# Kernel optimization log

Measured on AMD Instinct MI355X. Metric: run time of the kernel, lower is better.

## Reference

```python
import jax, jax.numpy as jnp
import numpy as np

B, D, H, F, L, M, MEM, ACT, STO, HID = 2048, 1024, 8, 4096, 2, 256, 16, 32, 1024, 1024
HD = D // H
SCALE = HD ** -0.5
EPS = 1e-4


def rmsnorm(x, w):
    return x * jax.lax.rsqrt(jnp.mean(x * x, axis=-1, keepdims=True) + EPS) * w


def setup_inputs() -> dict:
    key = jax.random.key(0)
    ks = iter(jax.random.split(key, 32))

    def nrm(shape, scale=0.02):
        return jax.random.normal(next(ks), shape, dtype=jnp.float32) * scale

    return {
        'stoch': jax.random.normal(next(ks), (B, STO), dtype=jnp.float32),
        'deter': jax.random.normal(next(ks), (B, D), dtype=jnp.float32),
        'action': jax.random.normal(next(ks), (B, ACT), dtype=jnp.float32),
        'memory': jax.random.normal(next(ks), (B, MEM, D), dtype=jnp.float32),
        'inp_w1': nrm((STO + ACT, HID)), 'inp_b1': jnp.zeros((HID,), jnp.float32),
        'inp_nw': jnp.ones((HID,), jnp.float32),
        'inp_w2': nrm((HID, D)), 'inp_b2': jnp.zeros((D,), jnp.float32),
        'Wq': nrm((L, D, D)), 'bq': jnp.zeros((L, D), jnp.float32),
        'Wk': nrm((L, D, D)), 'bk': jnp.zeros((L, D), jnp.float32),
        'Wv': nrm((L, D, D)), 'bv': jnp.zeros((L, D), jnp.float32),
        'Wo': nrm((L, D, D)), 'bo': jnp.zeros((L, D), jnp.float32),
        'rel_emb': nrm((L, 2 * M + 1, H)),
        'n1w': jnp.ones((L, D), jnp.float32), 'n2w': jnp.ones((L, D), jnp.float32),
        'ffw1': nrm((L, D, F)), 'ffb1': jnp.zeros((L, F), jnp.float32),
        'ffw2': nrm((L, F, D)), 'ffb2': jnp.zeros((L, D), jnp.float32),
        'fnw': jnp.ones((D,), jnp.float32),
    }


def reference(stoch, deter, action, memory, inp_w1, inp_b1, inp_nw, inp_w2, inp_b2,
              Wq, bq, Wk, bk, Wv, bv, Wo, bo, rel_emb, n1w, n2w,
              ffw1, ffb1, ffw2, ffb2, fnw):
    # action normalization: denominator is detached in torch
    a = action / jax.lax.stop_gradient(jnp.maximum(jnp.abs(action), 1.0))
    tok = jnp.concatenate([stoch.reshape(stoch.shape[0], -1), a], axis=-1)
    tok = jax.nn.silu(rmsnorm(tok @ inp_w1 + inp_b1, inp_nw)) @ inp_w2 + inp_b2  # [B,D]
    seq = jnp.concatenate([memory, tok[:, None, :]], axis=1)  # [B,S,D], S = MEM+1
    S = seq.shape[1]
    rel = jnp.clip(jnp.arange(S)[:, None] - jnp.arange(S)[None, :], -M, M) + M  # [S,S]
    for l in range(L):
        xn = rmsnorm(seq, n1w[l])
        q = (xn @ Wq[l] + bq[l]).reshape(-1, S, H, HD)
        k = (xn @ Wk[l] + bk[l]).reshape(-1, S, H, HD)
        v = (xn @ Wv[l] + bv[l]).reshape(-1, S, H, HD)
        bias = rel_emb[l][rel].transpose(2, 0, 1)  # [H,S,S]
        scores = jnp.einsum('bqhd,bkhd->bhqk', q, k) * SCALE + bias[None]
        probs = jax.nn.softmax(scores, axis=-1)
        att = jnp.einsum('bhqk,bkhd->bqhd', probs, v).reshape(-1, S, D)
        seq = seq + (att @ Wo[l] + bo[l])
        xn2 = rmsnorm(seq, n2w[l])
        seq = seq + (jax.nn.gelu(xn2 @ ffw1[l] + ffb1[l], approximate=False) @ ffw2[l] + ffb2[l])
    new_deter = rmsnorm(seq[:, -1] + deter, fnw)
    new_mem = jax.lax.stop_gradient(seq[:, -MEM:])
    return (new_deter, new_mem)
```

## Files before the change

kernel.cpp:

```cpp
#include <hip/hip_runtime.h>
#include <hip/hip_bf16.h>
#include <math.h>

#define NB 2048
#define ND 1024
#define NH 8
#define NHD 128
#define NF 4096
#define NL 2
#define NMEM 16
#define NS 17
#define NROWS (NB*NS)
#define NTOK 1056
#define SCALE_ATT 0.08838834764831845f

typedef unsigned short u16;
typedef unsigned int u32;

typedef __bf16 bf16x8 __attribute__((ext_vector_type(8)));
typedef float f32x4 __attribute__((ext_vector_type(4)));

__device__ __forceinline__ float bf2f(u16 h) {
  union { u32 u; float f; } c; c.u = ((u32)h) << 16; return c.f;
}
__device__ __forceinline__ u16 f2bf(float f) {
  union { float ff; u32 u; } c; c.ff = f;
  return (u16)((c.u + 0x7FFFu + ((c.u >> 16) & 1u)) >> 16);
}
__device__ __forceinline__ bf16x8 as_b8(uint4 u) {
  union { uint4 u; bf16x8 b; } c; c.u = u; return c.b;
}

__device__ __forceinline__ void gload16(const void* g, void* l) {
  __builtin_amdgcn_global_load_lds(
      (const __attribute__((address_space(1))) void*)(uintptr_t)g,
      (__attribute__((address_space(3))) void*)(u32)(uintptr_t)l,
      16, 0, 0);
}

__global__ __launch_bounds__(256)
void pack_wT_k(const float* __restrict__ src, u16* __restrict__ dst, int K, int N)
{
  __shared__ float tile[32][33];
  int tx = threadIdx.x & 31, ty = threadIdx.x >> 5;
  int n0 = blockIdx.x * 32, k0 = blockIdx.y * 32;
#pragma unroll
  for (int r = ty; r < 32; r += 8)
    tile[r][tx] = src[(size_t)(k0 + r) * N + n0 + tx];
  __syncthreads();
#pragma unroll
  for (int r = ty; r < 32; r += 8)
    dst[(size_t)(n0 + r) * K + k0 + tx] = f2bf(tile[tx][r]);
}

__global__ __launch_bounds__(256)
void pack_bqkv_k(const float* __restrict__ bq, const float* __restrict__ bk,
                 const float* __restrict__ bv, float* __restrict__ dst)
{
  int j = blockIdx.x * 256 + threadIdx.x;
  if (j >= 3072) return;
  float v = (j < 1024) ? bq[j] : (j < 2048 ? bk[j - 1024] : bv[j - 2048]);
  dst[j] = v;
}

template<int EPI>
__global__ __launch_bounds__(256)
void gemm2_k(const u16* __restrict__ A, int lda,
             const u16* __restrict__ BT, int ldb,
             const float* __restrict__ bias,
             u16* __restrict__ Cb, float* __restrict__ Cf, int ldc,
             int K)
{
  __shared__ __align__(16) u16 Asm[2][128 * 32];
  __shared__ __align__(16) u16 Bsm[2][128 * 32];
  const int tid  = threadIdx.x;
  const int lane = tid & 63;
  const int wv   = tid >> 6;
  const int wm   = wv >> 1, wn = wv & 1;
  const int lr   = lane & 15;
  const int kb   = lane >> 4;

  const int gx = gridDim.x;
  const int nwg = gx * gridDim.y;
  int bid = blockIdx.y * gx + blockIdx.x;
  if ((nwg & 7) == 0) bid = (bid & 7) * (nwg >> 3) + (bid >> 3);
  const int bx = bid % gx, by = bid / gx;
  const long bmBase = (long)by * 128;
  const int  bnBase = bx * 128;

  const int srow = tid >> 2;
  const int skc  = (tid & 3) * 8;
  const u16* aG0 = A  + (size_t)(bmBase + srow) * lda + skc;
  const u16* aG1 = aG0 + (size_t)64 * lda;
  const u16* bG0 = BT + (size_t)(bnBase + srow) * ldb + skc;
  const u16* bG1 = bG0 + (size_t)64 * ldb;
  const int wbase = (tid & ~63) * 8;

  f32x4 acc[4][4];
#pragma unroll
  for (int m = 0; m < 4; ++m)
#pragma unroll
    for (int n = 0; n < 4; ++n)
      acc[m][n] = (f32x4){0.0f, 0.0f, 0.0f, 0.0f};

  const int nk = K >> 5;

  {
    u16* aL = &Asm[0][wbase];
    u16* bL = &Bsm[0][wbase];
    gload16(aG0, aL);
    gload16(aG1, aL + 2048);
    gload16(bG0, bL);
    gload16(bG1, bL + 2048);
  }
  asm volatile("s_waitcnt vmcnt(0)" ::: "memory");
  __builtin_amdgcn_s_barrier();

  for (int i = 0; i < nk; ++i) {
    const int cur = i & 1;
    if (i + 1 < nk) {
      const int kt = (i + 1) << 5;
      u16* aL = &Asm[cur ^ 1][wbase];
      u16* bL = &Bsm[cur ^ 1][wbase];
      gload16(aG0 + kt, aL);
      gload16(aG1 + kt, aL + 2048);
      gload16(bG0 + kt, bL);
      gload16(bG1 + kt, bL + 2048);
    }

    bf16x8 af[4], bfv[4];
#pragma unroll
    for (int m = 0; m < 4; ++m)
      af[m] = as_b8(*(const uint4*)&Asm[cur][(wm * 64 + m * 16 + lr) * 32 + kb * 8]);
#pragma unroll
    for (int n = 0; n < 4; ++n)
      bfv[n] = as_b8(*(const uint4*)&Bsm[cur][(wn * 64 + n * 16 + lr) * 32 + kb * 8]);
#pragma unroll
    for (int m = 0; m < 4; ++m)
#pragma unroll
      for (int n = 0; n < 4; ++n)
        acc[m][n] = __builtin_amdgcn_mfma_f32_16x16x32_bf16(af[m], bfv[n], acc[m][n], 0, 0, 0);

    asm volatile("s_waitcnt vmcnt(0)" ::: "memory");
    __builtin_amdgcn_s_barrier();
  }

#pragma unroll
  for (int m = 0; m < 4; ++m) {
#pragma unroll
    for (int n = 0; n < 4; ++n) {
      int gcol = bnBase + wn * 64 + n * 16 + lr;
      float bv = bias[gcol];
      long growb = bmBase + wm * 64 + m * 16 + (lane >> 4) * 4;
#pragma unroll
      for (int i = 0; i < 4; ++i) {
        float val = acc[m][n][i] + bv;
        long row = growb + i;
        if (EPI == 1) val = 0.5f * val * (1.0f + erff(val * 0.70710678118654752f));
        if (EPI == 0 || EPI == 1) {
          Cb[(size_t)row * ldc + gcol] = f2bf(val);
        } else if (EPI == 2) {
          float* p = Cf + (size_t)row * ldc + gcol;
          *p = *p + val;
        } else {
          Cf[(size_t)row * ldc + gcol] = val;
        }
      }
    }
  }
}

__global__ __launch_bounds__(256)
void prep_tokcat_k(const float* __restrict__ stoch, const float* __restrict__ action,
                   u16* __restrict__ tok)
{
  size_t idx = (size_t)blockIdx.x * 256 + threadIdx.x;
  if (idx >= (size_t)NB * NTOK) return;
  int b = (int)(idx / NTOK), j = (int)(idx % NTOK);
  float v;
  if (j < 1024) {
    v = stoch[(size_t)b * 1024 + j];
  } else {
    float a = action[(size_t)b * 32 + (j - 1024)];
    v = a / fmaxf(fabsf(a), 1.0f);
  }
  tok[idx] = f2bf(v);
}

__global__ __launch_bounds__(256)
void rmsnorm_f32_k(const float* __restrict__ X, const float* __restrict__ w,
                   u16* __restrict__ Y)
{
  int row = blockIdx.x;
  const float* x = X + (size_t)row * 1024;
  int t = threadIdx.x;
  float4 v = *(const float4*)&x[t * 4];
  float ss = v.x * v.x + v.y * v.y + v.z * v.z + v.w * v.w;
#pragma unroll
  for (int o = 1; o < 64; o <<= 1) ss += __shfl_xor(ss, o, 64);
  __shared__ float red[4];
  if ((t & 63) == 0) red[t >> 6] = ss;
  __syncthreads();
  float tot = red[0] + red[1] + red[2] + red[3];
  float r = rsqrtf(tot * (1.0f / 1024.0f) + 1e-4f);
  float4 wv = *(const float4*)&w[t * 4];
  union { u16 s[4]; uint2 u; } ob;
  ob.s[0] = f2bf(v.x * r * wv.x);
  ob.s[1] = f2bf(v.y * r * wv.y);
  ob.s[2] = f2bf(v.z * r * wv.z);
  ob.s[3] = f2bf(v.w * r * wv.w);
  *(uint2*)&Y[(size_t)row * 1024 + t * 4] = ob.u;
}

__global__ __launch_bounds__(256)
void rmsnorm_silu_k(u16* __restrict__ X, const float* __restrict__ w)
{
  int row = blockIdx.x;
  u16* x = X + (size_t)row * 1024;
  int t = threadIdx.x;
  union { u16 s[4]; uint2 u; } iv;
  iv.u = *(uint2*)&x[t * 4];
  float v0 = bf2f(iv.s[0]), v1 = bf2f(iv.s[1]), v2 = bf2f(iv.s[2]), v3 = bf2f(iv.s[3]);
  float ss = v0 * v0 + v1 * v1 + v2 * v2 + v3 * v3;
#pragma unroll
  for (int o = 1; o < 64; o <<= 1) ss += __shfl_xor(ss, o, 64);
  __shared__ float red[4];
  if ((t & 63) == 0) red[t >> 6] = ss;
  __syncthreads();
  float tot = red[0] + red[1] + red[2] + red[3];
  float r = rsqrtf(tot * (1.0f / 1024.0f) + 1e-4f);
  float4 wv = *(const float4*)&w[t * 4];
  float n0 = v0 * r * wv.x;
  float n1 = v1 * r * wv.y;
  float n2 = v2 * r * wv.z;
  float n3 = v3 * r * wv.w;
  union { u16 s[4]; uint2 u; } ob;
  ob.s[0] = f2bf(n0 / (1.0f + expf(-n0)));
  ob.s[1] = f2bf(n1 / (1.0f + expf(-n1)));
  ob.s[2] = f2bf(n2 / (1.0f + expf(-n2)));
  ob.s[3] = f2bf(n3 / (1.0f + expf(-n3)));
  *(uint2*)&x[t * 4] = ob.u;
}

__global__ __launch_bounds__(256)
void init_seq_k(const float* __restrict__ mem, float* __restrict__ seq)
{
  size_t idx = ((size_t)blockIdx.x * 256 + threadIdx.x) * 4;
  if (idx >= (size_t)NB * 16 * 1024) return;
  size_t b = idx / (16 * 1024), rem = idx % (16 * 1024);
  float4 v = *(const float4*)&mem[idx];
  *(float4*)&seq[b * (size_t)NS * 1024 + rem] = v;
}

__global__ __launch_bounds__(256)
void copy_mem_k(const float* __restrict__ seq, float* __restrict__ out)
{
  size_t idx = ((size_t)blockIdx.x * 256 + threadIdx.x) * 4;
  if (idx >= (size_t)NB * 16 * 1024) return;
  size_t b = idx / (16 * 1024), rem = idx % (16 * 1024);
  float4 v = *(const float4*)&seq[b * (size_t)NS * 1024 + 1024 + rem];
  *(float4*)&out[idx] = v;
}

__global__ __launch_bounds__(256)
void final_deter_k(const float* __restrict__ seq, const float* __restrict__ deter,
                   const float* __restrict__ fnw, float* __restrict__ out)
{
  int b = blockIdx.x;
  const float* xs = seq + ((size_t)b * NS + 16) * 1024;
  const float* dt = deter + (size_t)b * 1024;
  int t = threadIdx.x;
  float v[4];
#pragma unroll
  for (int j = 0; j < 4; ++j) v[j] = xs[t * 4 + j] + dt[t * 4 + j];
  float ss = v[0] * v[0] + v[1] * v[1] + v[2] * v[2] + v[3] * v[3];
#pragma unroll
  for (int o = 1; o < 64; o <<= 1) ss += __shfl_xor(ss, o, 64);
  __shared__ float red[4];
  if ((t & 63) == 0) red[t >> 6] = ss;
  __syncthreads();
  float tot = red[0] + red[1] + red[2] + red[3];
  float r = rsqrtf(tot * (1.0f / 1024.0f) + 1e-4f);
  float4 ov;
  ov.x = v[0] * r * fnw[t * 4 + 0];
  ov.y = v[1] * r * fnw[t * 4 + 1];
  ov.z = v[2] * r * fnw[t * 4 + 2];
  ov.w = v[3] * r * fnw[t * 4 + 3];
  *(float4*)&out[(size_t)b * 1024 + t * 4] = ov;
}

#define LSTR 132
__global__ __launch_bounds__(256)
void attn_k(const u16* __restrict__ QKV, const float* __restrict__ rel,
            u16* __restrict__ O)
{
  __shared__ float qs[NS * LSTR];
  __shared__ float ks[NS * LSTR];
  __shared__ float vs[NS * LSTR];
  __shared__ float sc[NS * 20];
  int bh = blockIdx.x;
  int b = bh >> 3, h = bh & 7;
  int t = threadIdx.x;
  const size_t rowb = (size_t)b * NS * 3072 + h * 128;
  for (int e4 = t; e4 < NS * 32; e4 += 256) {
    int i = e4 >> 5, d = (e4 & 31) * 4;
    size_t off = rowb + (size_t)i * 3072 + d;
    uint2 q2 = *(const uint2*)(QKV + off);
    uint2 k2 = *(const uint2*)(QKV + off + 1024);
    uint2 v2 = *(const uint2*)(QKV + off + 2048);
    const u16* qp = (const u16*)&q2;
    const u16* kp = (const u16*)&k2;
    const u16* vp = (const u16*)&v2;
#pragma unroll
    for (int j = 0; j < 4; ++j) {
      qs[i * LSTR + d + j] = bf2f(qp[j]);
      ks[i * LSTR + d + j] = bf2f(kp[j]);
      vs[i * LSTR + d + j] = bf2f(vp[j]);
    }
  }
  __syncthreads();
  for (int e = t; e < NS * NS; e += 256) {
    int i = e / NS, j = e % NS;
    const float4* q4 = (const float4*)&qs[i * LSTR];
    const float4* k4 = (const float4*)&ks[j * LSTR];
    float s = 0.0f;
#pragma unroll
    for (int dd = 0; dd < 32; ++dd) {
      float4 a = q4[dd], bb = k4[dd];
      s += a.x * bb.x + a.y * bb.y + a.z * bb.z + a.w * bb.w;
    }
    sc[i * 20 + j] = s * SCALE_ATT + rel[(i - j + 256) * 8 + h];
  }
  __syncthreads();
  if (t < NS) {
    float mx = -1e30f;
    for (int j = 0; j < NS; ++j) mx = fmaxf(mx, sc[t * 20 + j]);
    float sum = 0.0f;
    for (int j = 0; j < NS; ++j) { float e = expf(sc[t * 20 + j] - mx); sc[t * 20 + j] = e; sum += e; }
    float inv = 1.0f / sum;
    for (int j = 0; j < NS; ++j) sc[t * 20 + j] *= inv;
  }
  __syncthreads();
  const size_t obase = (size_t)b * NS * 1024 + h * 128;
  for (int e = t; e < NS * 128; e += 256) {
    int i = e >> 7, d = e & 127;
    float o = 0.0f;
#pragma unroll
    for (int j = 0; j < NS; ++j) o += sc[i * 20 + j] * vs[j * LSTR + d];
    O[obase + (size_t)i * 1024 + d] = f2bf(o);
  }
}

extern "C" void kernel_launch(void* const* d_in, const int* in_sizes, int n_in,
                              void* d_out, int out_size, void* d_ws, size_t ws_size,
                              hipStream_t stream)
{
  const float* stoch  = (const float*)d_in[0];
  const float* deter  = (const float*)d_in[1];
  const float* action = (const float*)d_in[2];
  const float* memory = (const float*)d_in[3];
  const float* inp_w1 = (const float*)d_in[4];
  const float* inp_b1 = (const float*)d_in[5];
  const float* inp_nw = (const float*)d_in[6];
  const float* inp_w2 = (const float*)d_in[7];
  const float* inp_b2 = (const float*)d_in[8];
  const float* Wq = (const float*)d_in[9];
  const float* bq = (const float*)d_in[10];
  const float* Wk = (const float*)d_in[11];
  const float* bk = (const float*)d_in[12];
  const float* Wv = (const float*)d_in[13];
  const float* bv = (const float*)d_in[14];
  const float* Wo = (const float*)d_in[15];
  const float* bo = (const float*)d_in[16];
  const float* rel_emb = (const float*)d_in[17];
  const float* n1w = (const float*)d_in[18];
  const float* n2w = (const float*)d_in[19];
  const float* ffw1 = (const float*)d_in[20];
  const float* ffb1 = (const float*)d_in[21];
  const float* ffw2 = (const float*)d_in[22];
  const float* ffb2 = (const float*)d_in[23];
  const float* fnw  = (const float*)d_in[24];
  float* out = (float*)d_out;

  char* ws = (char*)d_ws;
  float* SEQ = (float*)ws;
  u16* XN  = (u16*)(ws + 142606336ULL);
  u16* QKV = (u16*)(ws + 213909504ULL);
  u16* FFH = QKV;
  u16* TOK = (u16*)(ws + 427819008ULL);
  u16* H1  = (u16*)(ws + 432144384ULL);
  u16* PK  = (u16*)(ws + 436338688ULL);
  float* BQKV = (float*)(ws + 461504512ULL);
  if (ws_size < 461516800ULL) return;

  dim3 blk(256);

  u16* w1T = PK;
  u16* w2T = PK + 1024 * 1056;
  pack_wT_k<<<dim3(1024 / 32, 1056 / 32), blk, 0, stream>>>(inp_w1, w1T, NTOK, 1024);
  pack_wT_k<<<dim3(1024 / 32, 1024 / 32), blk, 0, stream>>>(inp_w2, w2T, 1024, 1024);
  prep_tokcat_k<<<(NB * NTOK + 255) / 256, blk, 0, stream>>>(stoch, action, TOK);
  gemm2_k<0><<<dim3(8, 16), blk, 0, stream>>>(TOK, NTOK, w1T, NTOK, inp_b1, H1, nullptr, 1024, NTOK);
  rmsnorm_silu_k<<<NB, blk, 0, stream>>>(H1, inp_nw);
  gemm2_k<3><<<dim3(8, 16), blk, 0, stream>>>(H1, 1024, w2T, 1024, inp_b2, nullptr, SEQ + 16 * 1024, NS * 1024, 1024);
  init_seq_k<<<(NB * 16 * 1024 / 4 + 255) / 256, blk, 0, stream>>>(memory, SEQ);

  u16* qkvT = PK;
  u16* oT  = PK + 3145728;
  u16* f1T = PK + 4194304;
  u16* f2T = PK + 8388608;

  for (int l = 0; l < NL; ++l) {
    const float* wq = Wq + (size_t)l * ND * ND;
    const float* wk = Wk + (size_t)l * ND * ND;
    const float* wv = Wv + (size_t)l * ND * ND;
    const float* wo = Wo + (size_t)l * ND * ND;
    const float* w1 = ffw1 + (size_t)l * ND * NF;
    const float* w2 = ffw2 + (size_t)l * NF * ND;
    const float* rl = rel_emb + (size_t)l * 513 * NH;

    pack_wT_k<<<dim3(32, 32), blk, 0, stream>>>(wq, qkvT, 1024, 1024);
    pack_wT_k<<<dim3(32, 32), blk, 0, stream>>>(wk, qkvT + 1048576, 1024, 1024);
    pack_wT_k<<<dim3(32, 32), blk, 0, stream>>>(wv, qkvT + 2097152, 1024, 1024);
    pack_wT_k<<<dim3(32, 32), blk, 0, stream>>>(wo, oT, 1024, 1024);
    pack_wT_k<<<dim3(128, 32), blk, 0, stream>>>(w1, f1T, 1024, 4096);
    pack_wT_k<<<dim3(32, 128), blk, 0, stream>>>(w2, f2T, 4096, 1024);
    pack_bqkv_k<<<12, blk, 0, stream>>>(bq + l * ND, bk + l * ND, bv + l * ND, BQKV);

    rmsnorm_f32_k<<<NROWS, blk, 0, stream>>>(SEQ, n1w + l * ND, XN);
    gemm2_k<0><<<dim3(24, 272), blk, 0, stream>>>(XN, 1024, qkvT, 1024, BQKV, QKV, nullptr, 3072, 1024);
    attn_k<<<NB * NH, blk, 0, stream>>>(QKV, rl, XN);
    gemm2_k<2><<<dim3(8, 272), blk, 0, stream>>>(XN, 1024, oT, 1024, bo + l * ND, nullptr, SEQ, 1024, 1024);
    rmsnorm_f32_k<<<NROWS, blk, 0, stream>>>(SEQ, n2w + l * ND, XN);
    for (int c = 0; c < 2; ++c) {
      size_t r0 = (size_t)c * 17408;
      gemm2_k<1><<<dim3(32, 136), blk, 0, stream>>>(XN + r0 * 1024, 1024, f1T, 1024, ffb1 + l * NF, FFH, nullptr, 4096, 1024);
      gemm2_k<2><<<dim3(8, 136), blk, 0, stream>>>(FFH, 4096, f2T, 4096, ffb2 + l * ND, nullptr, SEQ + r0 * 1024, 1024, 4096);
    }
  }

  final_deter_k<<<NB, blk, 0, stream>>>(SEQ, deter, fnw, out);
  copy_mem_k<<<(NB * 16 * 1024 / 4 + 255) / 256, blk, 0, stream>>>(SEQ, out + (size_t)NB * ND);
}
```

Baseline: 3.469 ms.

## Add 256x256-tile 512-thread GEMM with swizzled LDS and XCD block remap

Adds a new GEMM kernel with 256x256 output tiles, 512 threads (8 waves each computing 128x64), a K-step of 64, and XOR-swizzled LDS layout to avoid bank conflicts. Block IDs are remapped across XCDs, and s_setprio is raised around the MFMA sequence. All layer GEMMs (QKV, output projection, FFN up/down) switch to it, aiming for more data reuse per loaded tile and less LDS traffic. The cost is higher register and LDS use (128KB LDS per block with double buffering), which may limit occupancy, and the larger tiles leave fewer blocks to spread across CUs.

```diff
diff --git a/kernel.cpp b/kernel.cpp
--- a/kernel.cpp
+++ b/kernel.cpp
@@ -104,7 +104,6 @@
       acc[m][n] = (f32x4){0.0f, 0.0f, 0.0f, 0.0f};
 
   const int nk = K >> 5;
-
   {
     u16* aL = &Asm[0][wbase];
     u16* bL = &Bsm[0][wbase];
@@ -127,7 +126,6 @@
       gload16(bG0 + kt, bL);
       gload16(bG1 + kt, bL + 2048);
     }
-
     bf16x8 af[4], bfv[4];
 #pragma unroll
     for (int m = 0; m < 4; ++m)
@@ -140,7 +138,6 @@
 #pragma unroll
       for (int n = 0; n < 4; ++n)
         acc[m][n] = __builtin_amdgcn_mfma_f32_16x16x32_bf16(af[m], bfv[n], acc[m][n], 0, 0, 0);
-
     asm volatile("s_waitcnt vmcnt(0)" ::: "memory");
     __builtin_amdgcn_s_barrier();
   }
@@ -164,6 +161,113 @@
           *p = *p + val;
         } else {
           Cf[(size_t)row * ldc + gcol] = val;
+        }
+      }
+    }
+  }
+}
+
+template<int EPI>
+__global__ __launch_bounds__(512, 2)
+void gemm3_k(const u16* __restrict__ A, int lda,
+             const u16* __restrict__ BT, int ldb,
+             const float* __restrict__ bias,
+             u16* __restrict__ Cb, float* __restrict__ Cf, int ldc,
+             int K)
+{
+  __shared__ __align__(16) u16 Ash[2][16384];
+  __shared__ __align__(16) u16 Bsh[2][16384];
+  const int tid  = threadIdx.x;
+  const int lane = tid & 63;
+  const int wv   = tid >> 6;
+  const int wm   = wv >> 2;
+  const int wn   = wv & 3;
+  const int lr   = lane & 15;
+  const int kb   = lane >> 4;
+
+  const int gx = gridDim.x;
+  const int nwg = gx * gridDim.y;
+  int bid = blockIdx.y * gx + blockIdx.x;
+  if ((nwg & 7) == 0) bid = (bid & 7) * (nwg >> 3) + (bid >> 3);
+  const int bx = bid % gx, by = bid / gx;
+  const long bmBase = (long)by * 256;
+  const int  bnBase = bx * 256;
+
+  const int r0 = tid >> 3;
+  const int xs = (((tid & 7) * 16) ^ ((r0 & 7) << 4)) >> 1;
+  const u16* aB = A  + (size_t)(bmBase + r0) * lda + xs;
+  const u16* bB = BT + (size_t)(bnBase + r0) * ldb + xs;
+  u16* aLd = &Ash[0][0] + tid * 8;
+  u16* bLd = &Bsh[0][0] + tid * 8;
+
+  f32x4 acc[8][4];
+#pragma unroll
+  for (int m = 0; m < 8; ++m)
+#pragma unroll
+    for (int n = 0; n < 4; ++n)
+      acc[m][n] = (f32x4){0.0f, 0.0f, 0.0f, 0.0f};
+
+  const int nt = K >> 6;
+
+#pragma unroll
+  for (int j = 0; j < 4; ++j) gload16(aB + (size_t)j * 64 * lda, aLd + j * 4096);
+#pragma unroll
+  for (int j = 0; j < 4; ++j) gload16(bB + (size_t)j * 64 * ldb, bLd + j * 4096);
+  asm volatile("s_waitcnt vmcnt(0)" ::: "memory");
+  __builtin_amdgcn_s_barrier();
+
+  for (int t = 0; t < nt; ++t) {
+    const int cur = t & 1;
+    if (t + 1 < nt) {
+      const int kt = (t + 1) << 6;
+      u16* aL = aLd + (cur ^ 1) * 16384;
+      u16* bL = bLd + (cur ^ 1) * 16384;
+#pragma unroll
+      for (int j = 0; j < 4; ++j) gload16(aB + kt + (size_t)j * 64 * lda, aL + j * 4096);
+#pragma unroll
+      for (int j = 0; j < 4; ++j) gload16(bB + kt + (size_t)j * 64 * ldb, bL + j * 4096);
+    }
+    const u16* As = &Ash[cur][0];
+    const u16* Bs = &Bsh[cur][0];
+#pragma unroll
+    for (int ks = 0; ks < 2; ++ks) {
+      const int kidx = (ks * 32 + kb * 8) ^ ((lr & 7) << 3);
+      bf16x8 af[8], bf[4];
+#pragma unroll
+      for (int m = 0; m < 8; ++m)
+        af[m] = as_b8(*(const uint4*)&As[(wm * 128 + m * 16 + lr) * 64 + kidx]);
+#pragma unroll
+      for (int n = 0; n < 4; ++n)
+        bf[n] = as_b8(*(const uint4*)&Bs[(wn * 64 + n * 16 + lr) * 64 + kidx]);
+      __builtin_amdgcn_s_setprio(1);
+#pragma unroll
+      for (int m = 0; m < 8; ++m)
+#pragma unroll
+        for (int n = 0; n < 4; ++n)
+          acc[m][n] = __builtin_amdgcn_mfma_f32_16x16x32_bf16(af[m], bf[n], acc[m][n], 0, 0, 0);
+      __builtin_amdgcn_s_setprio(0);
+    }
+    asm volatile("s_waitcnt vmcnt(0)" ::: "memory");
+    __builtin_amdgcn_s_barrier();
+  }
+
+#pragma unroll
+  for (int m = 0; m < 8; ++m) {
+#pragma unroll
+    for (int n = 0; n < 4; ++n) {
+      int gcol = bnBase + wn * 64 + n * 16 + lr;
+      float bv = bias[gcol];
+      long growb = bmBase + wm * 128 + m * 16 + (lane >> 4) * 4;
+#pragma unroll
+      for (int i = 0; i < 4; ++i) {
+        float val = acc[m][n][i] + bv;
+        long row = growb + i;
+        if (EPI == 1) val = 0.5f * val * (1.0f + erff(val * 0.70710678118654752f));
+        if (EPI == 0 || EPI == 1) {
+          Cb[(size_t)row * ldc + gcol] = f2bf(val);
+        } else {
+          float* p = Cf + (size_t)row * ldc + gcol;
+          *p = *p + val;
         }
       }
     }
@@ -394,6 +498,7 @@
   if (ws_size < 461516800ULL) return;
 
   dim3 blk(256);
+  dim3 blk5(512);
 
   u16* w1T = PK;
   u16* w2T = PK + 1024 * 1056;
@@ -428,14 +533,14 @@
     pack_bqkv_k<<<12, blk, 0, stream>>>(bq + l * ND, bk + l * ND, bv + l * ND, BQKV);
 
     rmsnorm_f32_k<<<NROWS, blk, 0, stream>>>(SEQ, n1w + l * ND, XN);
-    gemm2_k<0><<<dim3(24, 272), blk, 0, stream>>>(XN, 1024, qkvT, 1024, BQKV, QKV, nullptr, 3072, 1024);
+    gemm3_k<0><<<dim3(12, 136), blk5, 0, stream>>>(XN, 1024, qkvT, 1024, BQKV, QKV, nullptr, 3072, 1024);
     attn_k<<<NB * NH, blk, 0, stream>>>(QKV, rl, XN);
-    gemm2_k<2><<<dim3(8, 272), blk, 0, stream>>>(XN, 1024, oT, 1024, bo + l * ND, nullptr, SEQ, 1024, 1024);
+    gemm3_k<2><<<dim3(4, 136), blk5, 0, stream>>>(XN, 1024, oT, 1024, bo + l * ND, nullptr, SEQ, 1024, 1024);
     rmsnorm_f32_k<<<NROWS, blk, 0, stream>>>(SEQ, n2w + l * ND, XN);
     for (int c = 0; c < 2; ++c) {
       size_t r0 = (size_t)c * 17408;
-      gemm2_k<1><<<dim3(32, 136), blk, 0, stream>>>(XN + r0 * 1024, 1024, f1T, 1024, ffb1 + l * NF, FFH, nullptr, 4096, 1024);
-      gemm2_k<2><<<dim3(8, 136), blk, 0, stream>>>(FFH, 4096, f2T, 4096, ffb2 + l * ND, nullptr, SEQ + r0 * 1024, 1024, 4096);
+      gemm3_k<1><<<dim3(16, 68), blk5, 0, stream>>>(XN + r0 * 1024, 1024, f1T, 1024, ffb1 + l * NF, FFH, nullptr, 4096, 1024);
+      gemm3_k<2><<<dim3(4, 68), blk5, 0, stream>>>(FFH, 4096, f2T, 4096, ffb2 + l * ND, nullptr, SEQ + r0 * 1024, 1024, 4096);
     }
   }
 
```

New measurement: 4.044 ms. +16.6%, slower.
